# Performance work log

Measured on AMD Instinct MI355X. Metric: run time of the kernel, lower is better.

Reference implementation:

```python
import jax, jax.numpy as jnp
import numpy as np

B, T, C, H, WINDOW = 256, 1024, 128, 256, 24


def setup_inputs() -> dict:
    key = jax.random.key(0)
    ks = jax.random.split(key, 9)
    s = 1.0 / np.sqrt(H)  # torch LSTMCell uniform init scale
    return {
        "x": jax.random.normal(ks[0], (B, T, C), dtype=jnp.float32),
        "W_ih": jax.random.uniform(ks[1], (4 * H, C), jnp.float32, -s, s),
        "W_hh": jax.random.uniform(ks[2], (4 * H, H), jnp.float32, -s, s),
        "b_ih": jax.random.uniform(ks[3], (4 * H,), jnp.float32, -s, s),
        "b_hh": jax.random.uniform(ks[4], (4 * H,), jnp.float32, -s, s),
        "W_skip": jax.random.normal(ks[5], (H, H), dtype=jnp.float32) * np.sqrt(2.0 / (H + H)),
        "b_skip": jnp.zeros((H,), jnp.float32),
        "h0": jax.random.normal(ks[6], (1, H), dtype=jnp.float32) * np.sqrt(2.0 / (1 + H)),
        "c0": jax.random.normal(ks[7], (1, H), dtype=jnp.float32) * np.sqrt(2.0 / (1 + H)),
    }


def reference(x, W_ih, W_hh, b_ih, b_hh, W_skip, b_skip, h0, c0):
    Bb, Tt, _ = x.shape
    Hh = h0.shape[1]
    h = jnp.tile(h0, (Bb, 1))
    c = jnp.tile(c0, (Bb, 1))
    # ring buffer of the last WINDOW hidden states (output[i-WINDOW] lives at slot i % WINDOW)
    buf = jnp.zeros((WINDOW, Bb, Hh), x.dtype)
    # precompute the input contribution to the gates for all timesteps: [T, B, 4H]
    xg = jnp.einsum('btc,gc->tbg', x, W_ih) + b_ih + b_hh

    def step(carry, inp):
        h, c, buf = carry
        xg_t, i = inp
        idx = i % WINDOW
        skip = jax.lax.dynamic_index_in_dim(buf, idx, 0, keepdims=False)  # output[i-WINDOW]
        mask = (i >= WINDOW).astype(x.dtype)
        h_in = h + mask * (skip @ W_skip.T + b_skip)
        gates = xg_t + h_in @ W_hh.T  # [B, 4H]
        gi, gf, gg, go = jnp.split(gates, 4, axis=-1)  # torch order: i, f, g, o
        c_new = jax.nn.sigmoid(gf) * c + jax.nn.sigmoid(gi) * jnp.tanh(gg)
        h_new = jax.nn.sigmoid(go) * jnp.tanh(c_new)
        buf = jax.lax.dynamic_update_index_in_dim(buf, h_new, idx, 0)
        return (h_new, c_new, buf), h_new

    (h, c, _), out = jax.lax.scan(step, (h, c, buf), (xg, jnp.arange(Tt)))
    output = jnp.swapaxes(out, 0, 1)  # [B, T, H]
    return output, h, c
```

## Files before the change

### kernel.cpp

```cpp
#include <hip/hip_runtime.h>
#include <cstddef>
#include <cmath>

#define Bn  256
#define Tn  1024
#define Cn  128
#define Hn  256
#define WIN 24

#define NRG 16
#define NUG 16
#define RPB 16
#define UPB 16

#define AGENT __HIP_MEMORY_SCOPE_AGENT
#define RLX   __ATOMIC_RELAXED

typedef __attribute__((ext_vector_type(8))) short bf16x8;
typedef __attribute__((ext_vector_type(4))) float f32x4;
typedef __attribute__((ext_vector_type(4))) unsigned int u32x4;

#define MFMA(a, b, c) __builtin_amdgcn_mfma_f32_16x16x32_bf16((a), (b), (c), 0, 0, 0)

struct __align__(64) Flag { int v; int pad[15]; };
__device__ Flag g_flag[NRG][NUG];
__device__ unsigned short g_hx_hi[2][Bn][Hn];
__device__ unsigned short g_hx_lo[2][Bn][Hn];

__device__ inline unsigned short f2bf(float f) {
    union { float f; unsigned u; } v; v.f = f;
    unsigned r = (v.u + 0x7FFF + ((v.u >> 16) & 1)) >> 16;
    return (unsigned short)r;
}
__device__ inline float bf2f(unsigned short b) {
    union { unsigned u; float f; } v; v.u = (unsigned)b << 16;
    return v.f;
}
__device__ inline void split8(const float* s, bf16x8& hi, bf16x8& lo) {
    #pragma unroll
    for (int e = 0; e < 8; ++e) {
        unsigned short h = f2bf(s[e]);
        float r = s[e] - bf2f(h);
        hi[e] = (short)h;
        lo[e] = (short)f2bf(r);
    }
}
__device__ inline float fsigm(float x) {
    return __builtin_amdgcn_rcpf(1.f + exp2f(x * -1.442695041f));
}
__device__ inline float ftanh(float x) {
    return 1.f - 2.f * __builtin_amdgcn_rcpf(1.f + exp2f(x * 2.885390082f));
}

__global__ __launch_bounds__(256) void init_sync(const float* __restrict__ h0) {
    int i = blockIdx.x * 256 + threadIdx.x;
    int b = i >> 8, u = i & 255;
    float hv = h0[u];
    unsigned short hi = f2bf(hv);
    g_hx_hi[0][b][u] = hi;
    g_hx_lo[0][b][u] = f2bf(hv - bf2f(hi));
    g_hx_hi[1][b][u] = 0;
    g_hx_lo[1][b][u] = 0;
    if (i < NRG * NUG) g_flag[i >> 4][i & 15].v = 0;
}

__global__ __launch_bounds__(512, 1) void lstm_persist(
    const float* __restrict__ x,
    const float* __restrict__ W_ih, const float* __restrict__ W_hh,
    const float* __restrict__ b_ih, const float* __restrict__ b_hh,
    const float* __restrict__ W_skip, const float* __restrict__ b_skip,
    const float* __restrict__ h0, const float* __restrict__ c0,
    float* __restrict__ outp, float* __restrict__ hbuf, float* __restrict__ cbuf)
{
    __shared__ bf16x8 s_ga[2][12][64];
    __shared__ float  s_part[2][4][64][4];
    __shared__ float  s_sk[8][64][4];
    __shared__ __align__(16) unsigned short s_hown_hi[16][16];
    __shared__ __align__(16) unsigned short s_hown_lo[16][16];
    __shared__ float  s_hout[16][16];
    __shared__ float  s_bias[64];
    __shared__ float  s_bskip[UPB];
    __shared__ int    s_fl[16];
    __shared__ float  s_pad[9700];

    const int tid = threadIdx.x;
    if (tid == 0) ((volatile float*)s_pad)[0] = 0.f;

    const int xcd = blockIdx.x & 7, slot = blockIdx.x >> 3;
    const int rg = (xcd << 1) | (slot >> 4), ug = slot & 15;
    const int row0 = rg * RPB, u0 = ug * UPB;

    const int w = tid >> 6, lane = tid & 63;
    const int g = w & 3, kh = w >> 2;
    const int nl = lane & 15, kq = lane >> 4;
    const int sm = lane & 15;
    const int k0 = w * 32 + kq * 8;
    const int peer = k0 >> 4;
    const bool own = (peer == ug);
    const bool fw  = (w == 7) && (lane < 16);
    const int ksx2 = (tid >> 6) - 4, lx2 = tid & 63;
    const int mx2 = lx2 & 15, kqx2 = lx2 >> 4;

    bf16x8 whh_hi[4], whh_lo[4], wx_hi[2], wx_lo[2], ws_hi, ws_lo;
    {
        const int Rg = g * Hn + u0 + nl;
        const float* wr = W_hh + (size_t)Rg * Hn;
        #pragma unroll
        for (int j = 0; j < 4; ++j) {
            float tmp[8];
            const int k = (kh * 4 + j) * 32 + kq * 8;
            #pragma unroll
            for (int e = 0; e < 8; ++e) tmp[e] = wr[k + e];
            split8(tmp, whh_hi[j], whh_lo[j]);
        }
        const float* wr2 = W_ih + (size_t)Rg * Cn;
        #pragma unroll
        for (int j = 0; j < 2; ++j) {
            float tmp[8];
            const int k = (kh * 2 + j) * 32 + kq * 8;
            #pragma unroll
            for (int e = 0; e < 8; ++e) tmp[e] = wr2[k + e];
            split8(tmp, wx_hi[j], wx_lo[j]);
        }
        const float* wr3 = W_skip + (size_t)(u0 + nl) * Hn;
        float tmp[8];
        const int k = w * 32 + kq * 8;
        #pragma unroll
        for (int e = 0; e < 8; ++e) tmp[e] = wr3[k + e];
        split8(tmp, ws_hi, ws_lo);
    }
    if (tid < 64)  s_bias[tid]  = b_ih[(tid >> 4) * Hn + u0 + (tid & 15)]
                                + b_hh[(tid >> 4) * Hn + u0 + (tid & 15)];
    if (tid < 16)  s_bskip[tid] = b_skip[u0 + tid];

    float c_reg = 0.f;
    if (tid < 256) c_reg = c0[u0 + (tid & 15)];
    if (tid < 256) {
        float hv = h0[u0 + (tid & 15)];
        unsigned short phi = f2bf(hv);
        s_hown_hi[tid >> 4][tid & 15] = phi;
        s_hown_lo[tid >> 4][tid & 15] = f2bf(hv - bf2f(phi));
    }
    if (tid < 256) {
        const int ksx = tid >> 6, lx = tid & 63;
        const int mx = lx & 15, kqx = lx >> 4;
        const float* src = x + (size_t)(row0 + mx) * (Tn * Cn) + ksx * 32 + kqx * 8;
        float tmp[8];
        #pragma unroll
        for (int e = 0; e < 8; ++e) tmp[e] = src[e];
        bf16x8 hi, lo; split8(tmp, hi, lo);
        s_ga[0][ksx][lx] = hi; s_ga[1][ksx][lx] = lo;
    }
    f32x4 ring_a = {0.f,0.f,0.f,0.f}, ring_b = {0.f,0.f,0.f,0.f};
    __syncthreads();

    for (int t = 0; t < Tn; ++t) {
        const bool do_ring = (t >= WIN - 1) && (t < Tn - 1);
        const bool nr      = (t >= WIN - 2) && (t < Tn - 2);

        int f_s = 0;
        if (fw) f_s = __hip_atomic_load(&g_flag[rg][lane].v, RLX, AGENT);

        if (do_ring) {
            asm volatile("s_waitcnt vmcnt(0)" : "+v"(ring_a), "+v"(ring_b) :: "memory");
            float rvv[8];
            #pragma unroll
            for (int e = 0; e < 4; ++e) { rvv[e] = ring_a[e]; rvv[4 + e] = ring_b[e]; }
            bf16x8 hi, lo; split8(rvv, hi, lo);
            f32x4 sk0 = {0.f,0.f,0.f,0.f}, sk1 = {0.f,0.f,0.f,0.f}, sk2 = {0.f,0.f,0.f,0.f};
            sk0 = MFMA(hi, ws_hi, sk0);
            sk1 = MFMA(hi, ws_lo, sk1);
            sk2 = MFMA(lo, ws_hi, sk2);
            *(f32x4*)&s_sk[w][lane][0] = sk0 + sk1 + sk2;
        }
        if (fw) s_fl[lane] = f_s;
        __syncthreads();

        const unsigned short* hip_ = &g_hx_hi[t & 1][row0 + sm][k0];
        const unsigned short* lop_ = &g_hx_lo[t & 1][row0 + sm][k0];
        bf16x8 ha, hb;
        bool ready = false;
        if (!own && s_fl[peer] >= t) {
            ready = true;
            asm volatile("global_load_dwordx4 %0, %2, off sc0 sc1\n\t"
                         "global_load_dwordx4 %1, %3, off sc0 sc1"
                         : "=&v"(ha), "=&v"(hb) : "v"(hip_), "v"(lop_) : "memory");
        }

        f32x4 ac0 = {0.f,0.f,0.f,0.f}, ac1 = {0.f,0.f,0.f,0.f}, ac2 = {0.f,0.f,0.f,0.f};
        #pragma unroll
        for (int j = 0; j < 2; ++j) {
            const int ks = kh * 2 + j;
            bf16x8 ah = s_ga[0][ks][lane], al = s_ga[1][ks][lane];
            ac0 = MFMA(ah, wx_hi[j], ac0);
            ac1 = MFMA(ah, wx_lo[j], ac1);
            ac2 = MFMA(al, wx_hi[j], ac2);
        }

        if (!own && !ready) {
            int f2 = __hip_atomic_load(&g_flag[rg][peer].v, RLX, AGENT);
            if (f2 >= t) {
                ready = true;
                asm volatile("global_load_dwordx4 %0, %2, off sc0 sc1\n\t"
                             "global_load_dwordx4 %1, %3, off sc0 sc1"
                             : "=&v"(ha), "=&v"(hb) : "v"(hip_), "v"(lop_) : "memory");
            }
        }

        if (fw && f_s < t) {
            int f = f_s;
            while (f < t) f = __hip_atomic_load(&g_flag[rg][lane].v, RLX, AGENT);
        }
        __syncthreads();

        if (own) {
            bf16x8 hi8 = *(const bf16x8*)&s_hown_hi[sm][k0 & 15];
            bf16x8 lo8 = *(const bf16x8*)&s_hown_lo[sm][k0 & 15];
            s_ga[0][4 + w][lane] = hi8;
            s_ga[1][4 + w][lane] = lo8;
        } else {
            if (!ready) {
                asm volatile("global_load_dwordx4 %0, %2, off sc0 sc1\n\t"
                             "global_load_dwordx4 %1, %3, off sc0 sc1"
                             : "=&v"(ha), "=&v"(hb) : "v"(hip_), "v"(lop_) : "memory");
            }
            asm volatile("s_waitcnt vmcnt(0)" : "+v"(ha), "+v"(hb) :: "memory");
            s_ga[0][4 + w][lane] = ha;
            s_ga[1][4 + w][lane] = hb;
        }
        __syncthreads();

        f32x4 xa, xb;
        const bool xst = (tid >= 256) && (t + 1 < Tn);
        if (xst) {
            const float* xsrc = x + (size_t)(row0 + mx2) * (Tn * Cn)
                                  + (size_t)(t + 1) * Cn + ksx2 * 32 + kqx2 * 8;
            xa = *(const f32x4*)xsrc;
            xb = *(const f32x4*)(xsrc + 4);
        }
        #pragma unroll
        for (int j = 0; j < 4; ++j) {
            const int ks = 4 + kh * 4 + j;
            bf16x8 ah = s_ga[0][ks][lane], al = s_ga[1][ks][lane];
            ac0 = MFMA(ah, whh_hi[j], ac0);
            ac1 = MFMA(ah, whh_lo[j], ac1);
            ac2 = MFMA(al, whh_hi[j], ac2);
        }
        {
            f32x4 acc = ac0 + ac1 + ac2;
            *(f32x4*)&s_part[kh][g][lane][0] = acc;
        }
        __syncthreads();

        if (tid < 256) {
            const int m = tid >> 4, ul = tid & 15;
            const int li = ((m >> 2) << 4) | ul, r = m & 3;
            float gv[4];
            #pragma unroll
            for (int g2 = 0; g2 < 4; ++g2)
                gv[g2] = s_part[0][g2][li][r] + s_part[1][g2][li][r]
                       + s_bias[g2 * 16 + ul];
            float si = fsigm(gv[0]);
            float sf = fsigm(gv[1]);
            float gt = ftanh(gv[2]);
            float so = fsigm(gv[3]);
            c_reg = sf * c_reg + si * gt;
            float hn = so * ftanh(c_reg);
            s_hout[m][ul] = hn;
            if (t < Tn - 1) {
                float hin = hn;
                if (do_ring) {
                    float sk = 0.f;
                    #pragma unroll
                    for (int w2 = 0; w2 < 8; ++w2) sk += s_sk[w2][li][r];
                    hin += sk + s_bskip[ul];
                }
                unsigned short phi = f2bf(hin);
                s_hown_hi[m][ul] = phi;
                s_hown_lo[m][ul] = f2bf(hin - bf2f(phi));
            } else {
                hbuf[(size_t)(row0 + m) * Hn + u0 + ul] = hn;
                cbuf[(size_t)(row0 + m) * Hn + u0 + ul] = c_reg;
            }
        } else if (xst) {
            float tmp[8];
            #pragma unroll
            for (int e = 0; e < 4; ++e) { tmp[e] = xa[e]; tmp[4 + e] = xb[e]; }
            bf16x8 hi, lo; split8(tmp, hi, lo);
            s_ga[0][ksx2][lx2] = hi;
            s_ga[1][ksx2][lx2] = lo;
        }
        __syncthreads();

        if (t < Tn - 1) {
            if (tid < 32) {
                const int r8_ = tid >> 1, hf = tid & 1;
                u32x4 v = *(const u32x4*)&s_hown_hi[r8_][hf * 8];
                unsigned short* dst = &g_hx_hi[(t + 1) & 1][row0 + r8_][u0 + hf * 8];
                asm volatile("global_store_dwordx4 %0, %1, off sc0 sc1"
                             :: "v"(dst), "v"(v) : "memory");
            } else if (tid < 64) {
                const int r8_ = (tid - 32) >> 1, hf = tid & 1;
                u32x4 v = *(const u32x4*)&s_hown_lo[r8_][hf * 8];
                unsigned short* dst = &g_hx_lo[(t + 1) & 1][row0 + r8_][u0 + hf * 8];
                asm volatile("global_store_dwordx4 %0, %1, off sc0 sc1"
                             :: "v"(dst), "v"(v) : "memory");
            }
        }
        if (tid >= 64 && tid < 128) {
            const int r8_ = (tid - 64) >> 2, q = (tid - 64) & 3;
            f32x4 v = *(const f32x4*)&s_hout[r8_][q * 4];
            float* dst = &outp[(size_t)(row0 + r8_) * (Tn * Hn) + (size_t)t * Hn + u0 + q * 4];
            asm volatile("global_store_dwordx4 %0, %1, off sc0 sc1"
                         :: "v"(dst), "v"(v) : "memory");
        }
        asm volatile("s_waitcnt vmcnt(0)" ::: "memory");
        __syncthreads();
        if (t < Tn - 1) {
            if (tid == 0)
                __hip_atomic_store(&g_flag[rg][ug].v, t + 1, RLX, AGENT);
        }
        if (nr) {
            const float* rsrc = outp + (size_t)(row0 + sm) * (Tn * Hn)
                                     + (size_t)(t - (WIN - 2)) * Hn + k0;
            asm volatile("global_load_dwordx4 %0, %2, off sc0 sc1\n\t"
                         "global_load_dwordx4 %1, %2, off offset:16 sc0 sc1"
                         : "=&v"(ring_a), "=&v"(ring_b) : "v"(rsrc) : "memory");
        }
    }
}

extern "C" void kernel_launch(void* const* d_in, const int* in_sizes, int n_in,
                              void* d_out, int out_size, void* d_ws, size_t ws_size,
                              hipStream_t stream)
{
    const float* x      = (const float*)d_in[0];
    const float* W_ih   = (const float*)d_in[1];
    const float* W_hh   = (const float*)d_in[2];
    const float* b_ih   = (const float*)d_in[3];
    const float* b_hh   = (const float*)d_in[4];
    const float* W_skip = (const float*)d_in[5];
    const float* b_skip = (const float*)d_in[6];
    const float* h0     = (const float*)d_in[7];
    const float* c0     = (const float*)d_in[8];

    float* outp = (float*)d_out;
    float* hbuf = outp + (size_t)Bn * Tn * Hn;
    float* cbuf = hbuf + (size_t)Bn * Hn;

    init_sync<<<256, 256, 0, stream>>>(h0);
    lstm_persist<<<256, 512, 0, stream>>>(x, W_ih, W_hh, b_ih, b_hh,
                                          W_skip, b_skip, h0, c0, outp, hbuf, cbuf);
}
```

Before: 3.393 ms.

## Use per-wave flags and packed hi/lo hidden state to cut barriers

Packs the bf16 hi and lo halves of the hidden state into one 32-bit word, so each lane fetches its peer slice with one address pair. Replaces the single per-block flag with per-wave flags. Each finishing wave stores its h and output directly to global memory and publishes its own flag. Consumer lanes poll their specific producer flag instead of relying on one wave plus a block barrier. This removes two __syncthreads and the staged shared-memory store phase per timestep, double-buffering s_sk to avoid a hazard. The cost is finer-grained memory-ordering reasoning with a risk of subtle races, plus scalar rather than vectorized global stores.

```diff
diff --git a/kernel.cpp b/kernel.cpp
--- a/kernel.cpp
+++ b/kernel.cpp
@@ -1,6 +1,5 @@
 #include <hip/hip_runtime.h>
 #include <cstddef>
-#include <cmath>
 
 #define Bn  256
 #define Tn  1024
@@ -22,10 +21,8 @@
 
 #define MFMA(a, b, c) __builtin_amdgcn_mfma_f32_16x16x32_bf16((a), (b), (c), 0, 0, 0)
 
-struct __align__(64) Flag { int v; int pad[15]; };
-__device__ Flag g_flag[NRG][NUG];
-__device__ unsigned short g_hx_hi[2][Bn][Hn];
-__device__ unsigned short g_hx_lo[2][Bn][Hn];
+__device__ int g_flag2[NRG][NUG][16];
+__device__ unsigned g_hx_pk[2][Bn][Hn];
 
 __device__ inline unsigned short f2bf(float f) {
     union { float f; unsigned u; } v; v.f = f;
@@ -51,17 +48,21 @@
 __device__ inline float ftanh(float x) {
     return 1.f - 2.f * __builtin_amdgcn_rcpf(1.f + exp2f(x * 2.885390082f));
 }
+__device__ inline void ld_pk(const unsigned* p, u32x4& a, u32x4& b) {
+    asm volatile("global_load_dwordx4 %0, %2, off sc0 sc1\n\t"
+                 "global_load_dwordx4 %1, %2, off offset:16 sc0 sc1"
+                 : "=&v"(a), "=&v"(b) : "v"(p) : "memory");
+}
 
 __global__ __launch_bounds__(256) void init_sync(const float* __restrict__ h0) {
     int i = blockIdx.x * 256 + threadIdx.x;
     int b = i >> 8, u = i & 255;
     float hv = h0[u];
     unsigned short hi = f2bf(hv);
-    g_hx_hi[0][b][u] = hi;
-    g_hx_lo[0][b][u] = f2bf(hv - bf2f(hi));
-    g_hx_hi[1][b][u] = 0;
-    g_hx_lo[1][b][u] = 0;
-    if (i < NRG * NUG) g_flag[i >> 4][i & 15].v = 0;
+    unsigned short lo = f2bf(hv - bf2f(hi));
+    g_hx_pk[0][b][u] = ((unsigned)hi << 16) | lo;
+    g_hx_pk[1][b][u] = 0;
+    if (i < NRG * NUG * 16) ((int*)g_flag2)[i] = 0;
 }
 
 __global__ __launch_bounds__(512, 1) void lstm_persist(
@@ -72,16 +73,13 @@
     const float* __restrict__ h0, const float* __restrict__ c0,
     float* __restrict__ outp, float* __restrict__ hbuf, float* __restrict__ cbuf)
 {
-    __shared__ bf16x8 s_ga[2][12][64];
-    __shared__ float  s_part[2][4][64][4];
-    __shared__ float  s_sk[8][64][4];
-    __shared__ __align__(16) unsigned short s_hown_hi[16][16];
-    __shared__ __align__(16) unsigned short s_hown_lo[16][16];
-    __shared__ float  s_hout[16][16];
-    __shared__ float  s_bias[64];
-    __shared__ float  s_bskip[UPB];
-    __shared__ int    s_fl[16];
-    __shared__ float  s_pad[9700];
+    __shared__ bf16x8   s_ga[2][12][64];
+    __shared__ float    s_part[2][4][64][4];
+    __shared__ float    s_sk[2][8][64][4];
+    __shared__ unsigned s_hown_pk[16][16];
+    __shared__ float    s_bias[64];
+    __shared__ float    s_bskip[UPB];
+    __shared__ float    s_pad[7900];
 
     const int tid = threadIdx.x;
     if (tid == 0) ((volatile float*)s_pad)[0] = 0.f;
@@ -96,9 +94,9 @@
     const int sm = lane & 15;
     const int k0 = w * 32 + kq * 8;
     const int peer = k0 >> 4;
+    const int rqd  = sm >> 2;
     const bool own = (peer == ug);
-    const bool fw  = (w == 7) && (lane < 16);
-    const int ksx2 = (tid >> 6) - 4, lx2 = tid & 63;
+    const int ksx2 = w - 4, lx2 = lane;
     const int mx2 = lx2 & 15, kqx2 = lx2 >> 4;
 
     bf16x8 whh_hi[4], whh_lo[4], wx_hi[2], wx_lo[2], ws_hi, ws_lo;
@@ -134,12 +132,12 @@
     if (tid < 16)  s_bskip[tid] = b_skip[u0 + tid];
 
     float c_reg = 0.f;
-    if (tid < 256) c_reg = c0[u0 + (tid & 15)];
     if (tid < 256) {
+        c_reg = c0[u0 + (tid & 15)];
         float hv = h0[u0 + (tid & 15)];
         unsigned short phi = f2bf(hv);
-        s_hown_hi[tid >> 4][tid & 15] = phi;
-        s_hown_lo[tid >> 4][tid & 15] = f2bf(hv - bf2f(phi));
+        unsigned short plo = f2bf(hv - bf2f(phi));
+        s_hown_pk[tid >> 4][tid & 15] = ((unsigned)phi << 16) | plo;
     }
     if (tid < 256) {
         const int ksx = tid >> 6, lx = tid & 63;
@@ -152,14 +150,16 @@
         s_ga[0][ksx][lx] = hi; s_ga[1][ksx][lx] = lo;
     }
     f32x4 ring_a = {0.f,0.f,0.f,0.f}, ring_b = {0.f,0.f,0.f,0.f};
+    int* const fp = &g_flag2[rg][peer][rqd];
     __syncthreads();
 
     for (int t = 0; t < Tn; ++t) {
         const bool do_ring = (t >= WIN - 1) && (t < Tn - 1);
         const bool nr      = (t >= WIN - 2) && (t < Tn - 2);
-
-        int f_s = 0;
-        if (fw) f_s = __hip_atomic_load(&g_flag[rg][lane].v, RLX, AGENT);
+        const int  par     = t & 1;
+
+        int fv = 0x7fffffff;
+        if (!own) fv = __hip_atomic_load(fp, RLX, AGENT);
 
         if (do_ring) {
             asm volatile("s_waitcnt vmcnt(0)" : "+v"(ring_a), "+v"(ring_b) :: "memory");
@@ -171,21 +171,14 @@
             sk0 = MFMA(hi, ws_hi, sk0);
             sk1 = MFMA(hi, ws_lo, sk1);
             sk2 = MFMA(lo, ws_hi, sk2);
-            *(f32x4*)&s_sk[w][lane][0] = sk0 + sk1 + sk2;
-        }
-        if (fw) s_fl[lane] = f_s;
+            *(f32x4*)&s_sk[par][w][lane][0] = sk0 + sk1 + sk2;
+        }
         __syncthreads();
 
-        const unsigned short* hip_ = &g_hx_hi[t & 1][row0 + sm][k0];
-        const unsigned short* lop_ = &g_hx_lo[t & 1][row0 + sm][k0];
-        bf16x8 ha, hb;
-        bool ready = false;
-        if (!own && s_fl[peer] >= t) {
-            ready = true;
-            asm volatile("global_load_dwordx4 %0, %2, off sc0 sc1\n\t"
-                         "global_load_dwordx4 %1, %3, off sc0 sc1"
-                         : "=&v"(ha), "=&v"(hb) : "v"(hip_), "v"(lop_) : "memory");
-        }
+        const unsigned* pkp = &g_hx_pk[par][row0 + sm][k0];
+        u32x4 pa = {0,0,0,0}, pb = {0,0,0,0};
+        bool have = false;
+        if (!own && fv >= t) { ld_pk(pkp, pa, pb); have = true; }
 
         f32x4 ac0 = {0.f,0.f,0.f,0.f}, ac1 = {0.f,0.f,0.f,0.f}, ac2 = {0.f,0.f,0.f,0.f};
         #pragma unroll
@@ -197,47 +190,51 @@
             ac2 = MFMA(al, wx_hi[j], ac2);
         }
 
-        if (!own && !ready) {
-            int f2 = __hip_atomic_load(&g_flag[rg][peer].v, RLX, AGENT);
-            if (f2 >= t) {
-                ready = true;
-                asm volatile("global_load_dwordx4 %0, %2, off sc0 sc1\n\t"
-                             "global_load_dwordx4 %1, %3, off sc0 sc1"
-                             : "=&v"(ha), "=&v"(hb) : "v"(hip_), "v"(lop_) : "memory");
+        if (!own && !have) {
+            fv = __hip_atomic_load(fp, RLX, AGENT);
+            if (fv >= t) { ld_pk(pkp, pa, pb); have = true; }
+        }
+
+        {
+            bool need = (!own) && (fv < t);
+            while (__any(need)) {
+                if (need) {
+                    fv = __hip_atomic_load(fp, RLX, AGENT);
+                    need = fv < t;
+                }
             }
         }
-
-        if (fw && f_s < t) {
-            int f = f_s;
-            while (f < t) f = __hip_atomic_load(&g_flag[rg][lane].v, RLX, AGENT);
-        }
-        __syncthreads();
-
+        if (!own && !have) ld_pk(pkp, pa, pb);
+        asm volatile("s_waitcnt vmcnt(0)" : "+v"(pa), "+v"(pb) :: "memory");
         if (own) {
-            bf16x8 hi8 = *(const bf16x8*)&s_hown_hi[sm][k0 & 15];
-            bf16x8 lo8 = *(const bf16x8*)&s_hown_lo[sm][k0 & 15];
-            s_ga[0][4 + w][lane] = hi8;
-            s_ga[1][4 + w][lane] = lo8;
-        } else {
-            if (!ready) {
-                asm volatile("global_load_dwordx4 %0, %2, off sc0 sc1\n\t"
-                             "global_load_dwordx4 %1, %3, off sc0 sc1"
-                             : "=&v"(ha), "=&v"(hb) : "v"(hip_), "v"(lop_) : "memory");
+            #pragma unroll
+            for (int e = 0; e < 4; ++e) {
+                pa[e] = s_hown_pk[sm][(k0 & 15) + e];
+                pb[e] = s_hown_pk[sm][(k0 & 15) + 4 + e];
             }
-            asm volatile("s_waitcnt vmcnt(0)" : "+v"(ha), "+v"(hb) :: "memory");
-            s_ga[0][4 + w][lane] = ha;
-            s_ga[1][4 + w][lane] = hb;
-        }
-        __syncthreads();
-
+        }
+        {
+            union { bf16x8 v; unsigned d[4]; } Hh, Ll;
+            #pragma unroll
+            for (int e = 0; e < 2; ++e) {
+                Hh.d[e]     = (pa[2*e+1] & 0xFFFF0000u) | (pa[2*e] >> 16);
+                Ll.d[e]     = (pa[2*e+1] << 16)         | (pa[2*e] & 0xFFFFu);
+                Hh.d[2 + e] = (pb[2*e+1] & 0xFFFF0000u) | (pb[2*e] >> 16);
+                Ll.d[2 + e] = (pb[2*e+1] << 16)         | (pb[2*e] & 0xFFFFu);
+            }
+            s_ga[0][4 + w][lane] = Hh.v;
+            s_ga[1][4 + w][lane] = Ll.v;
+        }
         f32x4 xa, xb;
-        const bool xst = (tid >= 256) && (t + 1 < Tn);
+        const bool xst = (w >= 4) && (t + 1 < Tn);
         if (xst) {
             const float* xsrc = x + (size_t)(row0 + mx2) * (Tn * Cn)
                                   + (size_t)(t + 1) * Cn + ksx2 * 32 + kqx2 * 8;
             xa = *(const f32x4*)xsrc;
             xb = *(const f32x4*)(xsrc + 4);
         }
+        __syncthreads();
+
         #pragma unroll
         for (int j = 0; j < 4; ++j) {
             const int ks = 4 + kh * 4 + j;
@@ -266,19 +263,31 @@
             float so = fsigm(gv[3]);
             c_reg = sf * c_reg + si * gt;
             float hn = so * ftanh(c_reg);
-            s_hout[m][ul] = hn;
             if (t < Tn - 1) {
                 float hin = hn;
                 if (do_ring) {
                     float sk = 0.f;
                     #pragma unroll
-                    for (int w2 = 0; w2 < 8; ++w2) sk += s_sk[w2][li][r];
+                    for (int w2 = 0; w2 < 8; ++w2) sk += s_sk[par][w2][li][r];
                     hin += sk + s_bskip[ul];
                 }
                 unsigned short phi = f2bf(hin);
-                s_hown_hi[m][ul] = phi;
-                s_hown_lo[m][ul] = f2bf(hin - bf2f(phi));
+                unsigned short plo = f2bf(hin - bf2f(phi));
+                unsigned pk = ((unsigned)phi << 16) | plo;
+                unsigned* hdst = &g_hx_pk[par ^ 1][row0 + m][u0 + ul];
+                asm volatile("global_store_dword %0, %1, off sc0 sc1"
+                             :: "v"(hdst), "v"(pk) : "memory");
+                float* odst = &outp[(size_t)(row0 + m) * (Tn * Hn) + (size_t)t * Hn + u0 + ul];
+                asm volatile("global_store_dword %0, %1, off sc0 sc1"
+                             :: "v"(odst), "v"(hn) : "memory");
+                s_hown_pk[m][ul] = pk;
+                asm volatile("s_waitcnt vmcnt(1)" ::: "memory");
+                if ((tid & 63) == 0)
+                    __hip_atomic_store(&g_flag2[rg][ug][w], t + 1, RLX, AGENT);
             } else {
+                float* odst = &outp[(size_t)(row0 + m) * (Tn * Hn) + (size_t)t * Hn + u0 + ul];
+                asm volatile("global_store_dword %0, %1, off sc0 sc1"
+                             :: "v"(odst), "v"(hn) : "memory");
                 hbuf[(size_t)(row0 + m) * Hn + u0 + ul] = hn;
                 cbuf[(size_t)(row0 + m) * Hn + u0 + ul] = c_reg;
             }
@@ -290,36 +299,7 @@
             s_ga[0][ksx2][lx2] = hi;
             s_ga[1][ksx2][lx2] = lo;
         }
-        __syncthreads();
-
-        if (t < Tn - 1) {
-            if (tid < 32) {
-                const int r8_ = tid >> 1, hf = tid & 1;
-                u32x4 v = *(const u32x4*)&s_hown_hi[r8_][hf * 8];
-                unsigned short* dst = &g_hx_hi[(t + 1) & 1][row0 + r8_][u0 + hf * 8];
-                asm volatile("global_store_dwordx4 %0, %1, off sc0 sc1"
-                             :: "v"(dst), "v"(v) : "memory");
-            } else if (tid < 64) {
-                const int r8_ = (tid - 32) >> 1, hf = tid & 1;
-                u32x4 v = *(const u32x4*)&s_hown_lo[r8_][hf * 8];
-                unsigned short* dst = &g_hx_lo[(t + 1) & 1][row0 + r8_][u0 + hf * 8];
-                asm volatile("global_store_dwordx4 %0, %1, off sc0 sc1"
-                             :: "v"(dst), "v"(v) : "memory");
-            }
-        }
-        if (tid >= 64 && tid < 128) {
-            const int r8_ = (tid - 64) >> 2, q = (tid - 64) & 3;
-            f32x4 v = *(const f32x4*)&s_hout[r8_][q * 4];
-            float* dst = &outp[(size_t)(row0 + r8_) * (Tn * Hn) + (size_t)t * Hn + u0 + q * 4];
-            asm volatile("global_store_dwordx4 %0, %1, off sc0 sc1"
-                         :: "v"(dst), "v"(v) : "memory");
-        }
-        asm volatile("s_waitcnt vmcnt(0)" ::: "memory");
-        __syncthreads();
-        if (t < Tn - 1) {
-            if (tid == 0)
-                __hip_atomic_store(&g_flag[rg][ug].v, t + 1, RLX, AGENT);
-        }
+
         if (nr) {
             const float* rsrc = outp + (size_t)(row0 + sm) * (Tn * Hn)
                                      + (size_t)(t - (WIN - 2)) * Hn + k0;
```

New measurement: 4.668 ms. 1.38x slower.

## Halve grid by doubling hidden units per block and per-wave flag polling

Applied to the files above, without the earlier changes.

Each block now owns 32 hidden units instead of 16, so only 8 unit-groups per row group cooperate and the grid shrinks to 128 blocks. Each wave covers the full K range for one gate half instead of splitting K across wave pairs. That removes the cross-wave partial sum and one barrier per step. Flag polling moves from one dedicated wave to every non-owner wave polling its own peer, and the skip matmul is staged through shared memory. The change cuts cross-block synchronisation and global h exchange traffic, at the cost of more MFMA work and more weight registers per wave, and half the CUs left idle.

```diff
diff --git a/kernel.cpp b/kernel.cpp
--- a/kernel.cpp
+++ b/kernel.cpp
@@ -1,6 +1,5 @@
 #include <hip/hip_runtime.h>
 #include <cstddef>
-#include <cmath>
 
 #define Bn  256
 #define Tn  1024
@@ -9,16 +8,15 @@
 #define WIN 24
 
 #define NRG 16
-#define NUG 16
+#define NUG 8
 #define RPB 16
-#define UPB 16
+#define UPB 32
 
 #define AGENT __HIP_MEMORY_SCOPE_AGENT
 #define RLX   __ATOMIC_RELAXED
 
 typedef __attribute__((ext_vector_type(8))) short bf16x8;
 typedef __attribute__((ext_vector_type(4))) float f32x4;
-typedef __attribute__((ext_vector_type(4))) unsigned int u32x4;
 
 #define MFMA(a, b, c) __builtin_amdgcn_mfma_f32_16x16x32_bf16((a), (b), (c), 0, 0, 0)
 
@@ -61,7 +59,7 @@
     g_hx_lo[0][b][u] = f2bf(hv - bf2f(hi));
     g_hx_hi[1][b][u] = 0;
     g_hx_lo[1][b][u] = 0;
-    if (i < NRG * NUG) g_flag[i >> 4][i & 15].v = 0;
+    if (i < NRG * NUG) ((Flag*)g_flag)[i].v = 0;
 }
 
 __global__ __launch_bounds__(512, 1) void lstm_persist(
@@ -73,83 +71,85 @@
     float* __restrict__ outp, float* __restrict__ hbuf, float* __restrict__ cbuf)
 {
     __shared__ bf16x8 s_ga[2][12][64];
-    __shared__ float  s_part[2][4][64][4];
-    __shared__ float  s_sk[8][64][4];
-    __shared__ __align__(16) unsigned short s_hown_hi[16][16];
-    __shared__ __align__(16) unsigned short s_hown_lo[16][16];
-    __shared__ float  s_hout[16][16];
-    __shared__ float  s_bias[64];
+    __shared__ bf16x8 s_sa[2][8][64];
+    __shared__ float  s_part[8][64][4];
+    __shared__ float  s_sk[4][2][64][4];
+    __shared__ __align__(16) unsigned short s_hown_hi[16][32];
+    __shared__ __align__(16) unsigned short s_hown_lo[16][32];
+    __shared__ float  s_hout[16][32];
+    __shared__ float  s_bias[128];
     __shared__ float  s_bskip[UPB];
-    __shared__ int    s_fl[16];
-    __shared__ float  s_pad[9700];
+    __shared__ float  s_pad[5000];
 
     const int tid = threadIdx.x;
     if (tid == 0) ((volatile float*)s_pad)[0] = 0.f;
 
     const int xcd = blockIdx.x & 7, slot = blockIdx.x >> 3;
-    const int rg = (xcd << 1) | (slot >> 4), ug = slot & 15;
+    const int rg = (xcd << 1) | (slot >> 3), ug = slot & 7;
     const int row0 = rg * RPB, u0 = ug * UPB;
 
     const int w = tid >> 6, lane = tid & 63;
-    const int g = w & 3, kh = w >> 2;
+    const int g  = w >> 1, uh = w & 1;
     const int nl = lane & 15, kq = lane >> 4;
     const int sm = lane & 15;
     const int k0 = w * 32 + kq * 8;
-    const int peer = k0 >> 4;
-    const bool own = (peer == ug);
-    const bool fw  = (w == 7) && (lane < 16);
-    const int ksx2 = (tid >> 6) - 4, lx2 = tid & 63;
-    const int mx2 = lx2 & 15, kqx2 = lx2 >> 4;
-
-    bf16x8 whh_hi[4], whh_lo[4], wx_hi[2], wx_lo[2], ws_hi, ws_lo;
+    const bool own = (w == ug);
+    const int cm = tid >> 5, cu = tid & 31;
+    const int cli = ((cm >> 2) << 4) | (cu & 15), cr = cm & 3, cuh = cu >> 4;
+    const int ksx2 = w - 4;
+    const int mx2 = lane & 15, kqx2 = lane >> 4;
+
+    bf16x8 whh_hi[8], whh_lo[8], wx_hi[4], wx_lo[4], ws_hi[2], ws_lo[2];
     {
-        const int Rg = g * Hn + u0 + nl;
+        const int Rg = g * Hn + u0 + uh * 16 + nl;
         const float* wr = W_hh + (size_t)Rg * Hn;
+        #pragma unroll
+        for (int j = 0; j < 8; ++j) {
+            float tmp[8];
+            const int k = j * 32 + kq * 8;
+            #pragma unroll
+            for (int e = 0; e < 8; ++e) tmp[e] = wr[k + e];
+            split8(tmp, whh_hi[j], whh_lo[j]);
+        }
+        const float* wr2 = W_ih + (size_t)Rg * Cn;
         #pragma unroll
         for (int j = 0; j < 4; ++j) {
             float tmp[8];
-            const int k = (kh * 4 + j) * 32 + kq * 8;
-            #pragma unroll
-            for (int e = 0; e < 8; ++e) tmp[e] = wr[k + e];
-            split8(tmp, whh_hi[j], whh_lo[j]);
-        }
-        const float* wr2 = W_ih + (size_t)Rg * Cn;
+            const int k = j * 32 + kq * 8;
+            #pragma unroll
+            for (int e = 0; e < 8; ++e) tmp[e] = wr2[k + e];
+            split8(tmp, wx_hi[j], wx_lo[j]);
+        }
+        const int Rs = u0 + uh * 16 + nl;
+        const float* wr3 = W_skip + (size_t)Rs * Hn;
         #pragma unroll
         for (int j = 0; j < 2; ++j) {
             float tmp[8];
-            const int k = (kh * 2 + j) * 32 + kq * 8;
-            #pragma unroll
-            for (int e = 0; e < 8; ++e) tmp[e] = wr2[k + e];
-            split8(tmp, wx_hi[j], wx_lo[j]);
-        }
-        const float* wr3 = W_skip + (size_t)(u0 + nl) * Hn;
-        float tmp[8];
-        const int k = w * 32 + kq * 8;
-        #pragma unroll
-        for (int e = 0; e < 8; ++e) tmp[e] = wr3[k + e];
-        split8(tmp, ws_hi, ws_lo);
-    }
-    if (tid < 64)  s_bias[tid]  = b_ih[(tid >> 4) * Hn + u0 + (tid & 15)]
-                                + b_hh[(tid >> 4) * Hn + u0 + (tid & 15)];
-    if (tid < 16)  s_bskip[tid] = b_skip[u0 + tid];
-
-    float c_reg = 0.f;
-    if (tid < 256) c_reg = c0[u0 + (tid & 15)];
+            const int k = ((w >> 1) * 2 + j) * 32 + kq * 8;
+            #pragma unroll
+            for (int e = 0; e < 8; ++e) tmp[e] = wr3[k + e];
+            split8(tmp, ws_hi[j], ws_lo[j]);
+        }
+    }
+    if (tid < 128) s_bias[tid] = b_ih[(tid >> 5) * Hn + u0 + (tid & 31)]
+                               + b_hh[(tid >> 5) * Hn + u0 + (tid & 31)];
+    if (tid < UPB) s_bskip[tid] = b_skip[u0 + tid];
+
+    float c_reg = c0[u0 + cu];
+    {
+        float hv = h0[u0 + cu];
+        unsigned short phi = f2bf(hv);
+        s_hown_hi[cm][cu] = phi;
+        s_hown_lo[cm][cu] = f2bf(hv - bf2f(phi));
+    }
     if (tid < 256) {
-        float hv = h0[u0 + (tid & 15)];
-        unsigned short phi = f2bf(hv);
-        s_hown_hi[tid >> 4][tid & 15] = phi;
-        s_hown_lo[tid >> 4][tid & 15] = f2bf(hv - bf2f(phi));
-    }
-    if (tid < 256) {
-        const int ksx = tid >> 6, lx = tid & 63;
-        const int mx = lx & 15, kqx = lx >> 4;
-        const float* src = x + (size_t)(row0 + mx) * (Tn * Cn) + ksx * 32 + kqx * 8;
+        const int ksx = tid >> 6;
+        const float* src = x + (size_t)(row0 + sm) * (Tn * Cn) + ksx * 32 + kq * 8;
         float tmp[8];
         #pragma unroll
         for (int e = 0; e < 8; ++e) tmp[e] = src[e];
         bf16x8 hi, lo; split8(tmp, hi, lo);
-        s_ga[0][ksx][lx] = hi; s_ga[1][ksx][lx] = lo;
+        s_ga[0][ksx][lane] = hi; s_ga[1][ksx][lane] = lo;
     }
     f32x4 ring_a = {0.f,0.f,0.f,0.f}, ring_b = {0.f,0.f,0.f,0.f};
     __syncthreads();
@@ -157,9 +157,10 @@
     for (int t = 0; t < Tn; ++t) {
         const bool do_ring = (t >= WIN - 1) && (t < Tn - 1);
         const bool nr      = (t >= WIN - 2) && (t < Tn - 2);
-
-        int f_s = 0;
-        if (fw) f_s = __hip_atomic_load(&g_flag[rg][lane].v, RLX, AGENT);
+        const int  par     = t & 1;
+
+        int fv = 0x7fffffff;
+        if (!own) fv = __hip_atomic_load(&g_flag[rg][w].v, RLX, AGENT);
 
         if (do_ring) {
             asm volatile("s_waitcnt vmcnt(0)" : "+v"(ring_a), "+v"(ring_b) :: "memory");
@@ -167,21 +168,16 @@
             #pragma unroll
             for (int e = 0; e < 4; ++e) { rvv[e] = ring_a[e]; rvv[4 + e] = ring_b[e]; }
             bf16x8 hi, lo; split8(rvv, hi, lo);
-            f32x4 sk0 = {0.f,0.f,0.f,0.f}, sk1 = {0.f,0.f,0.f,0.f}, sk2 = {0.f,0.f,0.f,0.f};
-            sk0 = MFMA(hi, ws_hi, sk0);
-            sk1 = MFMA(hi, ws_lo, sk1);
-            sk2 = MFMA(lo, ws_hi, sk2);
-            *(f32x4*)&s_sk[w][lane][0] = sk0 + sk1 + sk2;
-        }
-        if (fw) s_fl[lane] = f_s;
-        __syncthreads();
-
-        const unsigned short* hip_ = &g_hx_hi[t & 1][row0 + sm][k0];
-        const unsigned short* lop_ = &g_hx_lo[t & 1][row0 + sm][k0];
+            s_sa[0][w][lane] = hi; s_sa[1][w][lane] = lo;
+        }
+        __syncthreads();
+
+        const unsigned short* hip_ = &g_hx_hi[par][row0 + sm][k0];
+        const unsigned short* lop_ = &g_hx_lo[par][row0 + sm][k0];
         bf16x8 ha, hb;
-        bool ready = false;
-        if (!own && s_fl[peer] >= t) {
-            ready = true;
+        bool have = false;
+        if (!own && fv >= t) {
+            have = true;
             asm volatile("global_load_dwordx4 %0, %2, off sc0 sc1\n\t"
                          "global_load_dwordx4 %1, %3, off sc0 sc1"
                          : "=&v"(ha), "=&v"(hb) : "v"(hip_), "v"(lop_) : "memory");
@@ -189,37 +185,38 @@
 
         f32x4 ac0 = {0.f,0.f,0.f,0.f}, ac1 = {0.f,0.f,0.f,0.f}, ac2 = {0.f,0.f,0.f,0.f};
         #pragma unroll
-        for (int j = 0; j < 2; ++j) {
-            const int ks = kh * 2 + j;
-            bf16x8 ah = s_ga[0][ks][lane], al = s_ga[1][ks][lane];
+        for (int j = 0; j < 4; ++j) {
+            bf16x8 ah = s_ga[0][j][lane], al = s_ga[1][j][lane];
             ac0 = MFMA(ah, wx_hi[j], ac0);
             ac1 = MFMA(ah, wx_lo[j], ac1);
             ac2 = MFMA(al, wx_hi[j], ac2);
         }
-
-        if (!own && !ready) {
-            int f2 = __hip_atomic_load(&g_flag[rg][peer].v, RLX, AGENT);
-            if (f2 >= t) {
-                ready = true;
+        if (do_ring) {
+            f32x4 sk0 = {0.f,0.f,0.f,0.f}, sk1 = {0.f,0.f,0.f,0.f}, sk2 = {0.f,0.f,0.f,0.f};
+            #pragma unroll
+            for (int j = 0; j < 2; ++j) {
+                const int ks = (w >> 1) * 2 + j;
+                bf16x8 ah = s_sa[0][ks][lane], al = s_sa[1][ks][lane];
+                sk0 = MFMA(ah, ws_hi[j], sk0);
+                sk1 = MFMA(ah, ws_lo[j], sk1);
+                sk2 = MFMA(al, ws_hi[j], sk2);
+            }
+            *(f32x4*)&s_sk[w >> 1][w & 1][lane][0] = sk0 + sk1 + sk2;
+        }
+        if (!own && !have) {
+            fv = __hip_atomic_load(&g_flag[rg][w].v, RLX, AGENT);
+            if (fv >= t) {
+                have = true;
                 asm volatile("global_load_dwordx4 %0, %2, off sc0 sc1\n\t"
                              "global_load_dwordx4 %1, %3, off sc0 sc1"
                              : "=&v"(ha), "=&v"(hb) : "v"(hip_), "v"(lop_) : "memory");
             }
         }
 
-        if (fw && f_s < t) {
-            int f = f_s;
-            while (f < t) f = __hip_atomic_load(&g_flag[rg][lane].v, RLX, AGENT);
-        }
-        __syncthreads();
-
-        if (own) {
-            bf16x8 hi8 = *(const bf16x8*)&s_hown_hi[sm][k0 & 15];
-            bf16x8 lo8 = *(const bf16x8*)&s_hown_lo[sm][k0 & 15];
-            s_ga[0][4 + w][lane] = hi8;
-            s_ga[1][4 + w][lane] = lo8;
-        } else {
-            if (!ready) {
+        if (!own) {
+            while (fv < t)
+                fv = __hip_atomic_load(&g_flag[rg][w].v, RLX, AGENT);
+            if (!have) {
                 asm volatile("global_load_dwordx4 %0, %2, off sc0 sc1\n\t"
                              "global_load_dwordx4 %1, %3, off sc0 sc1"
                              : "=&v"(ha), "=&v"(hb) : "v"(hip_), "v"(lop_) : "memory");
@@ -227,99 +224,95 @@
             asm volatile("s_waitcnt vmcnt(0)" : "+v"(ha), "+v"(hb) :: "memory");
             s_ga[0][4 + w][lane] = ha;
             s_ga[1][4 + w][lane] = hb;
-        }
-        __syncthreads();
-
+        } else {
+            s_ga[0][4 + w][lane] = *(const bf16x8*)&s_hown_hi[sm][kq * 8];
+            s_ga[1][4 + w][lane] = *(const bf16x8*)&s_hown_lo[sm][kq * 8];
+        }
         f32x4 xa, xb;
-        const bool xst = (tid >= 256) && (t + 1 < Tn);
+        const bool xst = (w >= 4) && (t + 1 < Tn);
         if (xst) {
             const float* xsrc = x + (size_t)(row0 + mx2) * (Tn * Cn)
                                   + (size_t)(t + 1) * Cn + ksx2 * 32 + kqx2 * 8;
             xa = *(const f32x4*)xsrc;
             xb = *(const f32x4*)(xsrc + 4);
         }
-        #pragma unroll
-        for (int j = 0; j < 4; ++j) {
-            const int ks = 4 + kh * 4 + j;
-            bf16x8 ah = s_ga[0][ks][lane], al = s_ga[1][ks][lane];
+        __syncthreads();
+
+        #pragma unroll
+        for (int j = 0; j < 8; ++j) {
+            bf16x8 ah = s_ga[0][4 + j][lane], al = s_ga[1][4 + j][lane];
             ac0 = MFMA(ah, whh_hi[j], ac0);
             ac1 = MFMA(ah, whh_lo[j], ac1);
             ac2 = MFMA(al, whh_hi[j], ac2);
         }
+        *(f32x4*)&s_part[w][lane][0] = ac0 + ac1 + ac2;
+        __syncthreads();
+
         {
-            f32x4 acc = ac0 + ac1 + ac2;
-            *(f32x4*)&s_part[kh][g][lane][0] = acc;
-        }
-        __syncthreads();
-
-        if (tid < 256) {
-            const int m = tid >> 4, ul = tid & 15;
-            const int li = ((m >> 2) << 4) | ul, r = m & 3;
             float gv[4];
             #pragma unroll
             for (int g2 = 0; g2 < 4; ++g2)
-                gv[g2] = s_part[0][g2][li][r] + s_part[1][g2][li][r]
-                       + s_bias[g2 * 16 + ul];
+                gv[g2] = s_part[g2 * 2 + cuh][cli][cr] + s_bias[g2 * 32 + cu];
             float si = fsigm(gv[0]);
             float sf = fsigm(gv[1]);
             float gt = ftanh(gv[2]);
             float so = fsigm(gv[3]);
             c_reg = sf * c_reg + si * gt;
             float hn = so * ftanh(c_reg);
-            s_hout[m][ul] = hn;
+            s_hout[cm][cu] = hn;
             if (t < Tn - 1) {
                 float hin = hn;
                 if (do_ring) {
-                    float sk = 0.f;
-                    #pragma unroll
-                    for (int w2 = 0; w2 < 8; ++w2) sk += s_sk[w2][li][r];
-                    hin += sk + s_bskip[ul];
+                    float sk = s_sk[0][cuh][cli][cr] + s_sk[1][cuh][cli][cr]
+                             + s_sk[2][cuh][cli][cr] + s_sk[3][cuh][cli][cr];
+                    hin += sk + s_bskip[cu];
                 }
                 unsigned short phi = f2bf(hin);
-                s_hown_hi[m][ul] = phi;
-                s_hown_lo[m][ul] = f2bf(hin - bf2f(phi));
+                s_hown_hi[cm][cu] = phi;
+                s_hown_lo[cm][cu] = f2bf(hin - bf2f(phi));
             } else {
-                hbuf[(size_t)(row0 + m) * Hn + u0 + ul] = hn;
-                cbuf[(size_t)(row0 + m) * Hn + u0 + ul] = c_reg;
-            }
+                hbuf[(size_t)(row0 + cm) * Hn + u0 + cu] = hn;
+                cbuf[(size_t)(row0 + cm) * Hn + u0 + cu] = c_reg;
+            }
+        }
+        __syncthreads();
+
+        if (tid < 64) {
+            if (t < Tn - 1) {
+                const int r8 = tid >> 2, q = tid & 3;
+                f32x4 v = *(const f32x4*)&s_hown_hi[r8][q * 8];
+                unsigned short* dst = &g_hx_hi[par ^ 1][row0 + r8][u0 + q * 8];
+                asm volatile("global_store_dwordx4 %0, %1, off sc0 sc1"
+                             :: "v"(dst), "v"(v) : "memory");
+            }
+        } else if (tid < 128) {
+            if (t < Tn - 1) {
+                const int r8 = (tid - 64) >> 2, q = tid & 3;
+                f32x4 v = *(const f32x4*)&s_hown_lo[r8][q * 8];
+                unsigned short* dst = &g_hx_lo[par ^ 1][row0 + r8][u0 + q * 8];
+                asm volatile("global_store_dwordx4 %0, %1, off sc0 sc1"
+                             :: "v"(dst), "v"(v) : "memory");
+            }
+        } else if (tid < 256) {
+            const int i = tid - 128, r8 = i >> 3, q = i & 7;
+            f32x4 v = *(const f32x4*)&s_hout[r8][q * 4];
+            float* dst = &outp[(size_t)(row0 + r8) * (Tn * Hn) + (size_t)t * Hn + u0 + q * 4];
+            asm volatile("global_store_dwordx4 %0, %1, off sc0 sc1"
+                         :: "v"(dst), "v"(v) : "memory");
         } else if (xst) {
             float tmp[8];
             #pragma unroll
             for (int e = 0; e < 4; ++e) { tmp[e] = xa[e]; tmp[4 + e] = xb[e]; }
             bf16x8 hi, lo; split8(tmp, hi, lo);
-            s_ga[0][ksx2][lx2] = hi;
-            s_ga[1][ksx2][lx2] = lo;
-        }
-        __syncthreads();
-
-        if (t < Tn - 1) {
-            if (tid < 32) {
-                const int r8_ = tid >> 1, hf = tid & 1;
-                u32x4 v = *(const u32x4*)&s_hown_hi[r8_][hf * 8];
-                unsigned short* dst = &g_hx_hi[(t + 1) & 1][row0 + r8_][u0 + hf * 8];
-                asm volatile("global_store_dwordx4 %0, %1, off sc0 sc1"
-                             :: "v"(dst), "v"(v) : "memory");
-            } else if (tid < 64) {
-                const int r8_ = (tid - 32) >> 1, hf = tid & 1;
-                u32x4 v = *(const u32x4*)&s_hown_lo[r8_][hf * 8];
-                unsigned short* dst = &g_hx_lo[(t + 1) & 1][row0 + r8_][u0 + hf * 8];
-                asm volatile("global_store_dwordx4 %0, %1, off sc0 sc1"
-                             :: "v"(dst), "v"(v) : "memory");
-            }
-        }
-        if (tid >= 64 && tid < 128) {
-            const int r8_ = (tid - 64) >> 2, q = (tid - 64) & 3;
-            f32x4 v = *(const f32x4*)&s_hout[r8_][q * 4];
-            float* dst = &outp[(size_t)(row0 + r8_) * (Tn * Hn) + (size_t)t * Hn + u0 + q * 4];
-            asm volatile("global_store_dwordx4 %0, %1, off sc0 sc1"
-                         :: "v"(dst), "v"(v) : "memory");
-        }
+            s_ga[0][ksx2][lane] = hi;
+            s_ga[1][ksx2][lane] = lo;
+        }
+
         asm volatile("s_waitcnt vmcnt(0)" ::: "memory");
         __syncthreads();
-        if (t < Tn - 1) {
-            if (tid == 0)
-                __hip_atomic_store(&g_flag[rg][ug].v, t + 1, RLX, AGENT);
-        }
+        if (t < Tn - 1 && tid == 0)
+            __hip_atomic_store(&g_flag[rg][ug].v, t + 1, RLX, AGENT);
+
         if (nr) {
             const float* rsrc = outp + (size_t)(row0 + sm) * (Tn * Hn)
                                      + (size_t)(t - (WIN - 2)) * Hn + k0;
@@ -349,6 +342,6 @@
     float* cbuf = hbuf + (size_t)Bn * Hn;
 
     init_sync<<<256, 256, 0, stream>>>(h0);
-    lstm_persist<<<256, 512, 0, stream>>>(x, W_ih, W_hh, b_ih, b_hh,
+    lstm_persist<<<128, 512, 0, stream>>>(x, W_ih, W_hh, b_ih, b_hh,
                                           W_skip, b_skip, h0, c0, outp, hbuf, cbuf);
 }
```

Result: faster. 3.184 ms (median of 2 runs) (-6.2%).
